# Kernel tuning notes

Hardware: AMD Instinct MI355X
Metric: run time of the kernel (lower is better)

## Reference

```python
import jax, jax.numpy as jnp
import numpy as np

TEMP = 0.5
EPS = 1e-8  # torch CosineSimilarity eps


def setup_inputs() -> dict:
    key = jax.random.key(0)
    k1, k2 = jax.random.split(key)
    B, D = 4096, 512
    z_i = jax.random.normal(k1, (B, D), dtype=jnp.float32)
    z_j = jax.random.normal(k2, (B, D), dtype=jnp.float32)
    return {"z_i": z_i, "z_j": z_j}


def reference(z_i, z_j):
    B = z_i.shape[0]
    N = 2 * B
    z = jnp.concatenate([z_i, z_j], axis=0)              # [N, D]
    norm = jnp.maximum(jnp.linalg.norm(z, axis=1, keepdims=True), EPS)
    zn = z / norm                                        # unit rows
    sim = jnp.matmul(zn, zn.T) / TEMP                    # [N, N] cosine sims / temperature
    # positives: sim[i, i+B] for i<B and sim[i+B, i] for i<B
    pos = jnp.concatenate([jnp.diagonal(sim, offset=B), jnp.diagonal(sim, offset=-B)])  # [N]
    # CE over logits [pos, negatives] with label 0 == -pos + logsumexp(row without diagonal)
    diag_mask = jnp.eye(N, dtype=bool)
    sim_masked = jnp.where(diag_mask, -jnp.inf, sim)
    lse = jax.nn.logsumexp(sim_masked, axis=1)           # [N]
    loss = jnp.sum(lse - pos) / N                        # CrossEntropyLoss(reduction='sum') / N
    return loss
```

## Files before the change

### kernel.cpp

```cpp
#include <hip/hip_runtime.h>
#include <stdint.h>

#define NROWS 8192
#define HALF_N 4096
#define DIM 512
#define INV_TEMP 2.0f

typedef __bf16 bf16x8 __attribute__((ext_vector_type(8)));
typedef float f32x4 __attribute__((ext_vector_type(4)));

__device__ __forceinline__ unsigned f2bf(float f) {
  unsigned u = __float_as_uint(f);
  unsigned r = 0x7FFFu + ((u >> 16) & 1u);
  return (u + r) >> 16;
}

__device__ __forceinline__ void gload_lds16(const unsigned short* g, unsigned short* l) {
  __builtin_amdgcn_global_load_lds(
      (const __attribute__((address_space(1))) unsigned int*)(uintptr_t)g,
      (__attribute__((address_space(3))) unsigned int*)(uint32_t)(uintptr_t)l,
      16, 0, 0);
}

__global__ void __launch_bounds__(256) k_normalize(const float* __restrict__ zi,
                                                   const float* __restrict__ zj,
                                                   unsigned short* __restrict__ zn,
                                                   float* __restrict__ sumexp) {
  int tid = threadIdx.x;
  int gid = blockIdx.x * 256 + tid;
  if (gid < NROWS) sumexp[gid] = 0.0f;
  int wave = tid >> 6, lane = tid & 63;
  int row = blockIdx.x * 4 + wave;
  const float* src = (row < HALF_N) ? (zi + (size_t)row * DIM)
                                    : (zj + (size_t)(row - HALF_N) * DIM);
  const float4* s4 = (const float4*)src;
  float4 a = s4[lane];
  float4 b = s4[lane + 64];
  float ss = a.x * a.x + a.y * a.y + a.z * a.z + a.w * a.w +
             b.x * b.x + b.y * b.y + b.z * b.z + b.w * b.w;
#pragma unroll
  for (int off = 32; off > 0; off >>= 1) ss += __shfl_xor(ss, off, 64);
  float nrm = fmaxf(sqrtf(ss), 1e-8f);
  float inv = 1.0f / nrm;
  uint2 oa, ob;
  oa.x = f2bf(a.x * inv) | (f2bf(a.y * inv) << 16);
  oa.y = f2bf(a.z * inv) | (f2bf(a.w * inv) << 16);
  ob.x = f2bf(b.x * inv) | (f2bf(b.y * inv) << 16);
  ob.y = f2bf(b.z * inv) | (f2bf(b.w * inv) << 16);
  unsigned short* dst = zn + (size_t)row * DIM;
  *((uint2*)(dst + lane * 4)) = oa;
  *((uint2*)(dst + 256 + lane * 4)) = ob;
}

__global__ void __launch_bounds__(256) k_simsum(const unsigned short* __restrict__ zn,
                                                float* __restrict__ sumexp,
                                                float* __restrict__ posv) {
  __shared__ __align__(16) unsigned short As[2][128 * 32];
  __shared__ __align__(16) unsigned short Bs[2][128 * 32];
  int tid = threadIdx.x;
  int wave = tid >> 6, lane = tid & 63;

  int idx = blockIdx.x;
  int tn = (int)((sqrtf(8.0f * idx + 1.0f) - 1.0f) * 0.5f);
  while (tn * (tn + 1) / 2 > idx) tn--;
  while ((tn + 1) * (tn + 2) / 2 <= idx) tn++;
  int tm = idx - tn * (tn + 1) / 2;
  int rowBase = tm * 128, colBase = tn * 128;
  int wr = (wave >> 1) * 64, wc = (wave & 1) * 64;
  int r15 = lane & 15, q = lane >> 4;

  int rA = wave * 32 + (lane >> 2);
  int swzS = (rA >> 1) & 3;
  int c8 = ((lane & 3) ^ swzS) * 8;
  const unsigned short* gA0 = zn + (size_t)(rowBase + rA) * DIM + c8;
  const unsigned short* gA1 = gA0 + 16 * DIM;
  const unsigned short* gB0 = zn + (size_t)(colBase + rA) * DIM + c8;
  const unsigned short* gB1 = gB0 + 16 * DIM;
  unsigned short* lA[2] = {&As[0][wave * 1024], &As[1][wave * 1024]};
  unsigned short* lB[2] = {&Bs[0][wave * 1024], &Bs[1][wave * 1024]};

#define STAGE(b)                         \
  do {                                   \
    gload_lds16(gA0, lA[b]);             \
    gload_lds16(gA1, lA[b] + 512);       \
    gload_lds16(gB0, lB[b]);             \
    gload_lds16(gB1, lB[b] + 512);       \
    gA0 += 32; gA1 += 32; gB0 += 32; gB1 += 32; \
  } while (0)

  f32x4 acc[4][4];
#pragma unroll
  for (int i = 0; i < 4; i++)
#pragma unroll
    for (int j = 0; j < 4; j++) acc[i][j] = (f32x4){0.f, 0.f, 0.f, 0.f};

  int swzR = (r15 >> 1) & 3;
  int aIdx0 = (wr + r15) * 4 + (q ^ swzR);
  int bIdx0 = (wc + r15) * 4 + (q ^ swzR);

#define COMPUTE(b)                                                               \
  do {                                                                           \
    const bf16x8* Av = (const bf16x8*)As[b];                                     \
    const bf16x8* Bv = (const bf16x8*)Bs[b];                                     \
    bf16x8 af[4], bfr[4];                                                        \
    _Pragma("unroll") for (int i = 0; i < 4; i++) af[i] = Av[aIdx0 + i * 64];    \
    _Pragma("unroll") for (int j = 0; j < 4; j++) bfr[j] = Bv[bIdx0 + j * 64];   \
    _Pragma("unroll") for (int i = 0; i < 4; i++)                                \
      _Pragma("unroll") for (int j = 0; j < 4; j++)                              \
        acc[i][j] = __builtin_amdgcn_mfma_f32_16x16x32_bf16(af[i], bfr[j], acc[i][j], 0, 0, 0); \
  } while (0)

  STAGE(0);
#pragma unroll
  for (int s = 0; s < 16; s += 2) {
    __syncthreads();
    if (s + 1 < 16) STAGE(1);
    COMPUTE(0);
    __syncthreads();
    if (s + 2 < 16) STAGE(0);
    COMPUTE(1);
  }

  bool isDiag = (tm == tn);
  bool hasPos = (tn == tm + 32);
  int gr0 = rowBase + wr + q * 4;
  int gc0 = colBase + wc + r15;
  float rs[16], cs[4];
#pragma unroll
  for (int t = 0; t < 16; t++) rs[t] = 0.f;
#pragma unroll
  for (int t = 0; t < 4; t++) cs[t] = 0.f;
#pragma unroll
  for (int i = 0; i < 4; i++) {
#pragma unroll
    for (int j = 0; j < 4; j++) {
#pragma unroll
      for (int r = 0; r < 4; r++) {
        float s = acc[i][j][r] * INV_TEMP;
        int gr = gr0 + i * 16 + r;
        int gc = gc0 + j * 16;
        if (hasPos && gc == gr + HALF_N) { posv[gr] = s; posv[gc] = s; }
        float e = __expf(s);
        if (isDiag && gc == gr) e = 0.f;
        rs[i * 4 + r] += e;
        cs[j] += e;
      }
    }
  }
#pragma unroll
  for (int t = 0; t < 8; t++) {
    float mine = (lane & 8) ? rs[t + 8] : rs[t];
    float oth = __shfl_xor((lane & 8) ? rs[t] : rs[t + 8], 8, 64);
    rs[t] = mine + oth;
  }
#pragma unroll
  for (int t = 0; t < 4; t++) {
    float mine = (lane & 4) ? rs[t + 4] : rs[t];
    float oth = __shfl_xor((lane & 4) ? rs[t] : rs[t + 4], 4, 64);
    rs[t] = mine + oth;
  }
#pragma unroll
  for (int t = 0; t < 2; t++) {
    float mine = (lane & 2) ? rs[t + 2] : rs[t];
    float oth = __shfl_xor((lane & 2) ? rs[t] : rs[t + 2], 2, 64);
    rs[t] = mine + oth;
  }
  {
    float mine = (lane & 1) ? rs[1] : rs[0];
    float oth = __shfl_xor((lane & 1) ? rs[0] : rs[1], 1, 64);
    rs[0] = mine + oth;
  }
  int myrow = rowBase + wr + q * 4 + ((r15 >> 2) * 16) + (r15 & 3);
  atomicAdd(&sumexp[myrow], rs[0]);

  if (!isDiag) {
#pragma unroll
    for (int t = 0; t < 2; t++) {
      float mine = (lane & 16) ? cs[t + 2] : cs[t];
      float oth = __shfl_xor((lane & 16) ? cs[t] : cs[t + 2], 16, 64);
      cs[t] = mine + oth;
    }
    {
      float mine = (lane & 32) ? cs[1] : cs[0];
      float oth = __shfl_xor((lane & 32) ? cs[0] : cs[1], 32, 64);
      cs[0] = mine + oth;
    }
    int myj = 2 * ((lane >> 4) & 1) + ((lane >> 5) & 1);
    atomicAdd(&sumexp[colBase + wc + myj * 16 + r15], cs[0]);
  }
#undef STAGE
#undef COMPUTE
}

__global__ void __launch_bounds__(1024) k_final(const float* __restrict__ sumexp,
                                                const float* __restrict__ posv,
                                                float* __restrict__ out) {
  __shared__ float red[16];
  int tid = threadIdx.x;
  const float4* se4 = (const float4*)sumexp;
  const float4* pv4 = (const float4*)posv;
  float p = 0.f;
#pragma unroll
  for (int c = 0; c < 2; c++) {
    float4 se = se4[tid * 2 + c];
    float4 pv = pv4[tid * 2 + c];
    p += (__logf(se.x) - pv.x) + (__logf(se.y) - pv.y) +
         (__logf(se.z) - pv.z) + (__logf(se.w) - pv.w);
  }
#pragma unroll
  for (int off = 32; off > 0; off >>= 1) p += __shfl_xor(p, off, 64);
  int wv = tid >> 6, ln = tid & 63;
  if (ln == 0) red[wv] = p;
  __syncthreads();
  if (tid == 0) {
    float t = 0.f;
    for (int w = 0; w < 16; w++) t += red[w];
    out[0] = t / (float)NROWS;
  }
}

extern "C" void kernel_launch(void* const* d_in, const int* in_sizes, int n_in,
                              void* d_out, int out_size, void* d_ws, size_t ws_size,
                              hipStream_t stream) {
  const float* zi = (const float*)d_in[0];
  const float* zj = (const float*)d_in[1];
  unsigned short* zn = (unsigned short*)d_ws;
  float* sumexp = (float*)((char*)d_ws + (size_t)NROWS * DIM * 2);
  float* posv = sumexp + NROWS;
  float* out = (float*)d_out;

  hipLaunchKernelGGL(k_normalize, dim3(2048), dim3(256), 0, stream, zi, zj, zn, sumexp);
  hipLaunchKernelGGL(k_simsum, dim3(2080), dim3(256), 0, stream, zn, sumexp, posv);
  hipLaunchKernelGGL(k_final, dim3(1), dim3(1024), 0, stream, sumexp, posv, out);
}
```

Before: 114.6 us.

## Double K-tile depth, fuse final reduction via last-block counter, use exp2

The K step per stage grows from 32 to 64 with a new 8-way XOR swizzle, which halves the number of barrier and stage iterations. Diagonal masking and positive extraction now run only on the lanes that hold diagonal entries, and exp uses exp2 with a folded scale. The separate final kernel is removed. The last block to finish, found through an atomic counter reset in the normalize kernel, computes the loss. This saves a launch, but it doubles LDS per block and relies on threadfence ordering between the atomics.

```diff
diff --git a/kernel.cpp b/kernel.cpp
--- a/kernel.cpp
+++ b/kernel.cpp
@@ -5,6 +5,8 @@
 #define HALF_N 4096
 #define DIM 512
 #define INV_TEMP 2.0f
+#define E2SCALE 2.8853900817779268f
+#define LN2 0.6931471805599453f
 
 typedef __bf16 bf16x8 __attribute__((ext_vector_type(8)));
 typedef float f32x4 __attribute__((ext_vector_type(4)));
@@ -25,10 +27,12 @@
 __global__ void __launch_bounds__(256) k_normalize(const float* __restrict__ zi,
                                                    const float* __restrict__ zj,
                                                    unsigned short* __restrict__ zn,
-                                                   float* __restrict__ sumexp) {
+                                                   float* __restrict__ sumexp,
+                                                   int* __restrict__ counter) {
   int tid = threadIdx.x;
   int gid = blockIdx.x * 256 + tid;
   if (gid < NROWS) sumexp[gid] = 0.0f;
+  if (gid == 0) *counter = 0;
   int wave = tid >> 6, lane = tid & 63;
   int row = blockIdx.x * 4 + wave;
   const float* src = (row < HALF_N) ? (zi + (size_t)row * DIM)
@@ -52,11 +56,13 @@
   *((uint2*)(dst + 256 + lane * 4)) = ob;
 }
 
-__global__ void __launch_bounds__(256) k_simsum(const unsigned short* __restrict__ zn,
-                                                float* __restrict__ sumexp,
-                                                float* __restrict__ posv) {
-  __shared__ __align__(16) unsigned short As[2][128 * 32];
-  __shared__ __align__(16) unsigned short Bs[2][128 * 32];
+__global__ void __launch_bounds__(256, 2) k_simsum(const unsigned short* __restrict__ zn,
+                                                   float* __restrict__ sumexp,
+                                                   float* __restrict__ posv,
+                                                   int* __restrict__ counter,
+                                                   float* __restrict__ out) {
+  __shared__ __align__(16) unsigned short As[2][128 * 64];
+  __shared__ __align__(16) unsigned short Bs[2][128 * 64];
   int tid = threadIdx.x;
   int wave = tid >> 6, lane = tid & 63;
 
@@ -69,23 +75,24 @@
   int wr = (wave >> 1) * 64, wc = (wave & 1) * 64;
   int r15 = lane & 15, q = lane >> 4;
 
-  int rA = wave * 32 + (lane >> 2);
-  int swzS = (rA >> 1) & 3;
-  int c8 = ((lane & 3) ^ swzS) * 8;
-  const unsigned short* gA0 = zn + (size_t)(rowBase + rA) * DIM + c8;
-  const unsigned short* gA1 = gA0 + 16 * DIM;
-  const unsigned short* gB0 = zn + (size_t)(colBase + rA) * DIM + c8;
-  const unsigned short* gB1 = gB0 + 16 * DIM;
-  unsigned short* lA[2] = {&As[0][wave * 1024], &As[1][wave * 1024]};
-  unsigned short* lB[2] = {&Bs[0][wave * 1024], &Bs[1][wave * 1024]};
-
-#define STAGE(b)                         \
-  do {                                   \
-    gload_lds16(gA0, lA[b]);             \
-    gload_lds16(gA1, lA[b] + 512);       \
-    gload_lds16(gB0, lB[b]);             \
-    gload_lds16(gB1, lB[b] + 512);       \
-    gA0 += 32; gA1 += 32; gB0 += 32; gB1 += 32; \
+  int rgrp = lane >> 3;
+  int xcol = (lane & 7) ^ rgrp;
+  const unsigned short* gA = zn + (size_t)(rowBase + wave * 32 + rgrp) * DIM + xcol * 8;
+  const unsigned short* gB = zn + (size_t)(colBase + wave * 32 + rgrp) * DIM + xcol * 8;
+  unsigned short* lA[2] = {&As[0][wave * 2048], &As[1][wave * 2048]};
+  unsigned short* lB[2] = {&Bs[0][wave * 2048], &Bs[1][wave * 2048]};
+
+#define STAGE(b)                                   \
+  do {                                             \
+    gload_lds16(gA, lA[b]);                        \
+    gload_lds16(gA + 8 * DIM, lA[b] + 512);        \
+    gload_lds16(gA + 16 * DIM, lA[b] + 1024);      \
+    gload_lds16(gA + 24 * DIM, lA[b] + 1536);      \
+    gload_lds16(gB, lB[b]);                        \
+    gload_lds16(gB + 8 * DIM, lB[b] + 512);        \
+    gload_lds16(gB + 16 * DIM, lB[b] + 1024);      \
+    gload_lds16(gB + 24 * DIM, lB[b] + 1536);      \
+    gA += 64; gB += 64;                            \
   } while (0)
 
   f32x4 acc[4][4];
@@ -94,59 +101,72 @@
 #pragma unroll
     for (int j = 0; j < 4; j++) acc[i][j] = (f32x4){0.f, 0.f, 0.f, 0.f};
 
-  int swzR = (r15 >> 1) & 3;
-  int aIdx0 = (wr + r15) * 4 + (q ^ swzR);
-  int bIdx0 = (wc + r15) * 4 + (q ^ swzR);
-
-#define COMPUTE(b)                                                               \
-  do {                                                                           \
-    const bf16x8* Av = (const bf16x8*)As[b];                                     \
-    const bf16x8* Bv = (const bf16x8*)Bs[b];                                     \
-    bf16x8 af[4], bfr[4];                                                        \
-    _Pragma("unroll") for (int i = 0; i < 4; i++) af[i] = Av[aIdx0 + i * 64];    \
-    _Pragma("unroll") for (int j = 0; j < 4; j++) bfr[j] = Bv[bIdx0 + j * 64];   \
-    _Pragma("unroll") for (int i = 0; i < 4; i++)                                \
-      _Pragma("unroll") for (int j = 0; j < 4; j++)                              \
-        acc[i][j] = __builtin_amdgcn_mfma_f32_16x16x32_bf16(af[i], bfr[j], acc[i][j], 0, 0, 0); \
+  int sw8 = r15 & 7;
+  int aOff = (wr + r15) * 8;
+  int bOff = (wc + r15) * 8;
+
+#define COMPUTE(b)                                                                   \
+  do {                                                                               \
+    const bf16x8* Av = (const bf16x8*)As[b];                                         \
+    const bf16x8* Bv = (const bf16x8*)Bs[b];                                         \
+    _Pragma("unroll") for (int t = 0; t < 2; t++) {                                  \
+      int g = (t * 4 + q) ^ sw8;                                                     \
+      bf16x8 af[4], bfr[4];                                                          \
+      _Pragma("unroll") for (int i = 0; i < 4; i++) af[i] = Av[aOff + i * 128 + g];  \
+      _Pragma("unroll") for (int j = 0; j < 4; j++) bfr[j] = Bv[bOff + j * 128 + g]; \
+      _Pragma("unroll") for (int i = 0; i < 4; i++)                                  \
+        _Pragma("unroll") for (int j = 0; j < 4; j++)                                \
+          acc[i][j] = __builtin_amdgcn_mfma_f32_16x16x32_bf16(af[i], bfr[j],         \
+                                                              acc[i][j], 0, 0, 0);   \
+    }                                                                                \
   } while (0)
 
   STAGE(0);
 #pragma unroll
-  for (int s = 0; s < 16; s += 2) {
+  for (int s = 0; s < 8; s += 2) {
     __syncthreads();
-    if (s + 1 < 16) STAGE(1);
+    if (s + 1 < 8) STAGE(1);
     COMPUTE(0);
     __syncthreads();
-    if (s + 2 < 16) STAGE(0);
+    if (s + 2 < 8) STAGE(0);
     COMPUTE(1);
   }
 
   bool isDiag = (tm == tn);
   bool hasPos = (tn == tm + 32);
-  int gr0 = rowBase + wr + q * 4;
-  int gc0 = colBase + wc + r15;
+  int rsel = r15 & 3;
+  bool diagLane = (wr == wc) && (q == (r15 >> 2));
+
+  if (isDiag && diagLane) {
+#pragma unroll
+    for (int i = 0; i < 4; i++) acc[i][i][rsel] = -1e30f;
+  }
+  if (hasPos && diagLane) {
+#pragma unroll
+    for (int i = 0; i < 4; i++) {
+      float s = acc[i][i][rsel] * INV_TEMP;
+      int gr = rowBase + wr + i * 16 + r15;
+      __hip_atomic_store(&posv[gr], s, __ATOMIC_RELAXED, __HIP_MEMORY_SCOPE_AGENT);
+      __hip_atomic_store(&posv[gr + HALF_N], s, __ATOMIC_RELAXED, __HIP_MEMORY_SCOPE_AGENT);
+    }
+  }
+
   float rs[16], cs[4];
 #pragma unroll
   for (int t = 0; t < 16; t++) rs[t] = 0.f;
 #pragma unroll
   for (int t = 0; t < 4; t++) cs[t] = 0.f;
 #pragma unroll
-  for (int i = 0; i < 4; i++) {
-#pragma unroll
-    for (int j = 0; j < 4; j++) {
+  for (int i = 0; i < 4; i++)
+#pragma unroll
+    for (int j = 0; j < 4; j++)
 #pragma unroll
       for (int r = 0; r < 4; r++) {
-        float s = acc[i][j][r] * INV_TEMP;
-        int gr = gr0 + i * 16 + r;
-        int gc = gc0 + j * 16;
-        if (hasPos && gc == gr + HALF_N) { posv[gr] = s; posv[gc] = s; }
-        float e = __expf(s);
-        if (isDiag && gc == gr) e = 0.f;
+        float e = __builtin_amdgcn_exp2f(acc[i][j][r] * E2SCALE);
         rs[i * 4 + r] += e;
         cs[j] += e;
       }
-    }
-  }
+
 #pragma unroll
   for (int t = 0; t < 8; t++) {
     float mine = (lane & 8) ? rs[t + 8] : rs[t];
@@ -170,7 +190,7 @@
     float oth = __shfl_xor((lane & 1) ? rs[0] : rs[1], 1, 64);
     rs[0] = mine + oth;
   }
-  int myrow = rowBase + wr + q * 4 + ((r15 >> 2) * 16) + (r15 & 3);
+  int myrow = rowBase + wr + ((r15 >> 2) * 16) + q * 4 + (r15 & 3);
   atomicAdd(&sumexp[myrow], rs[0]);
 
   if (!isDiag) {
@@ -188,35 +208,31 @@
     int myj = 2 * ((lane >> 4) & 1) + ((lane >> 5) & 1);
     atomicAdd(&sumexp[colBase + wc + myj * 16 + r15], cs[0]);
   }
+
+  __threadfence();
+  __shared__ int amLast;
+  if (tid == 0) {
+    int prev = __hip_atomic_fetch_add(counter, 1, __ATOMIC_ACQ_REL, __HIP_MEMORY_SCOPE_AGENT);
+    amLast = (prev == (int)gridDim.x - 1);
+  }
+  __syncthreads();
+  if (amLast) {
+    __threadfence();
+    float p = 0.f;
+    for (int r = tid; r < NROWS; r += 256) {
+      float se = __hip_atomic_load(&sumexp[r], __ATOMIC_RELAXED, __HIP_MEMORY_SCOPE_AGENT);
+      float pv = __hip_atomic_load(&posv[r], __ATOMIC_RELAXED, __HIP_MEMORY_SCOPE_AGENT);
+      p += __builtin_amdgcn_logf(se) * LN2 - pv;
+    }
+#pragma unroll
+    for (int off = 32; off > 0; off >>= 1) p += __shfl_xor(p, off, 64);
+    __shared__ float red[4];
+    if (lane == 0) red[wave] = p;
+    __syncthreads();
+    if (tid == 0) out[0] = (red[0] + red[1] + red[2] + red[3]) / (float)NROWS;
+  }
 #undef STAGE
 #undef COMPUTE
-}
-
-__global__ void __launch_bounds__(1024) k_final(const float* __restrict__ sumexp,
-                                                const float* __restrict__ posv,
-                                                float* __restrict__ out) {
-  __shared__ float red[16];
-  int tid = threadIdx.x;
-  const float4* se4 = (const float4*)sumexp;
-  const float4* pv4 = (const float4*)posv;
-  float p = 0.f;
-#pragma unroll
-  for (int c = 0; c < 2; c++) {
-    float4 se = se4[tid * 2 + c];
-    float4 pv = pv4[tid * 2 + c];
-    p += (__logf(se.x) - pv.x) + (__logf(se.y) - pv.y) +
-         (__logf(se.z) - pv.z) + (__logf(se.w) - pv.w);
-  }
-#pragma unroll
-  for (int off = 32; off > 0; off >>= 1) p += __shfl_xor(p, off, 64);
-  int wv = tid >> 6, ln = tid & 63;
-  if (ln == 0) red[wv] = p;
-  __syncthreads();
-  if (tid == 0) {
-    float t = 0.f;
-    for (int w = 0; w < 16; w++) t += red[w];
-    out[0] = t / (float)NROWS;
-  }
 }
 
 extern "C" void kernel_launch(void* const* d_in, const int* in_sizes, int n_in,
@@ -227,9 +243,9 @@
   unsigned short* zn = (unsigned short*)d_ws;
   float* sumexp = (float*)((char*)d_ws + (size_t)NROWS * DIM * 2);
   float* posv = sumexp + NROWS;
+  int* counter = (int*)(posv + NROWS);
   float* out = (float*)d_out;
 
-  hipLaunchKernelGGL(k_normalize, dim3(2048), dim3(256), 0, stream, zi, zj, zn, sumexp);
-  hipLaunchKernelGGL(k_simsum, dim3(2080), dim3(256), 0, stream, zn, sumexp, posv);
-  hipLaunchKernelGGL(k_final, dim3(1), dim3(1024), 0, stream, sumexp, posv, out);
-}
+  hipLaunchKernelGGL(k_normalize, dim3(2048), dim3(256), 0, stream, zi, zj, zn, sumexp, counter);
+  hipLaunchKernelGGL(k_simsum, dim3(2080), dim3(256), 0, stream, zn, sumexp, posv, counter, out);
+}
```

New measurement: 278.6 us. 143% more time.
